# Kernel optimization log

Hardware: AMD Instinct MI355X
Metric: run time of the kernel (lower is better)

## Reference

```python
import jax, jax.numpy as jnp
import numpy as np

NEG_INF = jnp.float32(-1e30)


def setup_inputs() -> dict:
    key = jax.random.key(0)
    ks = jax.random.split(key, 7)
    B, Lx, Lm, d = 4, 256, 256, 256
    return {
        "x": jax.random.normal(ks[0], (B, Lx, d), dtype=jnp.float32),
        "memory": jax.random.normal(ks[1], (B, Lm, d), dtype=jnp.float32),
        "memory_mask": jax.random.randint(ks[2], (B, Lm), 0, 2, dtype=jnp.int32),
        "ws1_w": jax.random.normal(ks[3], (d, d), dtype=jnp.float32) * 0.05,
        "ws1_b": jax.random.normal(ks[4], (d,), dtype=jnp.float32) * 0.05,
        "ws2_w": jax.random.normal(ks[5], (d, d), dtype=jnp.float32) * 0.05,
        "wst_w": jax.random.normal(ks[6], (1, d), dtype=jnp.float32) * 0.05,
    }


def reference(x, memory, memory_mask, ws1_w, ws1_b, ws2_w, wst_w):
    # x: [B, Lx, d], memory: [B, Lm, d]; torch Linear: y = x @ W.T + b
    item1 = jnp.einsum('bxd,ed->bxe', x, ws1_w) + ws1_b          # [B, Lx, d]
    item2 = jnp.einsum('bmd,ed->bme', memory, ws2_w)             # [B, Lm, d]
    item = jnp.tanh(item1[:, :, None, :] + item2[:, None, :, :])  # [B, Lx, Lm, d]
    S = jnp.einsum('bxmd,d->bxm', item, wst_w[0])                # [B, Lx, Lm]
    # agg_2_h uses the UNMASKED scores, softmax over Lx after transpose
    agg_2_h = jnp.einsum('bmx,bxd->bmd', jax.nn.softmax(S.transpose(0, 2, 1), axis=-1), x)
    # mask applied to S before the main attention readout
    S = jnp.where(memory_mask[:, None, :] == 0, NEG_INF, S)      # [B, Lx, Lm]
    out = jnp.einsum('bxm,bmd->bxd', jax.nn.softmax(S, axis=-1), memory)
    return (out, S, agg_2_h)
```

## Files before the change

kernel.cpp:

```cpp
#include <hip/hip_runtime.h>

static constexpr int NB = 4;
static constexpr int L  = 256;
static constexpr int D  = 256;

__device__ __forceinline__ float fast_rcp(float x) {
#if __has_builtin(__builtin_amdgcn_rcpf)
    return __builtin_amdgcn_rcpf(x);
#else
    return 1.0f / x;
#endif
}

__device__ __forceinline__ float fast_exp(float x) {
#if __has_builtin(__builtin_amdgcn_exp2f)
    return __builtin_amdgcn_exp2f(x * 1.4426950408889634f);
#else
    return __expf(x);
#endif
}

__device__ __forceinline__ float exp_2x(float x) {
#if __has_builtin(__builtin_amdgcn_exp2f)
    return __builtin_amdgcn_exp2f(x * 2.8853900817779268f);
#else
    return __expf(2.0f * x);
#endif
}

__device__ __forceinline__ float tanh_from_e(float e) {
    return fmaf(-2.0f, fast_rcp(e + 1.0f), 1.0f);
}

__global__ __launch_bounds__(256) void linear_kernel(
    const float* __restrict__ x, const float* __restrict__ mem,
    const float* __restrict__ w1, const float* __restrict__ b1,
    const float* __restrict__ w2,
    float* __restrict__ E1X, float* __restrict__ E2X)
{
    const int bid = blockIdx.x;
    const int rb  = (bid >> 3) * 32;
    const int cb  = (bid & 7) * 32;
    const int which = rb >= 1024;
    const int rloc  = which ? rb - 1024 : rb;
    const float* src = which ? mem : x;
    const float* W   = which ? w2  : w1;
    float*       dstX = which ? E2X : E1X;

    constexpr int P4 = 65;
    __shared__ __align__(16) float4 xs4[32 * P4];
    __shared__ __align__(16) float4 ws4[32 * P4];

    const int t = threadIdx.x;
    const float4* src4 = reinterpret_cast<const float4*>(src) + rloc * 64;
    const float4* Wg4  = reinterpret_cast<const float4*>(W)   + cb   * 64;
#pragma unroll
    for (int k = 0; k < 8; ++k) {
        int idx = k * 256 + t;
        int r = idx >> 6, c = idx & 63;
        xs4[r * P4 + c] = src4[r * 64 + c];
        ws4[r * P4 + c] = Wg4[r * 64 + c];
    }
    __syncthreads();

    const int rr = t >> 4, cc = t & 15;
    const float4* a0p = xs4 + rr * P4;
    const float4* a1p = xs4 + (rr + 16) * P4;
    const float4* w0p = ws4 + cc * P4;
    const float4* w1p = ws4 + (cc + 16) * P4;
    float acc00 = 0.f, acc01 = 0.f, acc10 = 0.f, acc11 = 0.f;
#pragma unroll 4
    for (int d4 = 0; d4 < 64; ++d4) {
        float4 a0 = a0p[d4], a1 = a1p[d4];
        float4 w0 = w0p[d4], w1 = w1p[d4];
        acc00 = fmaf(a0.x, w0.x, acc00); acc00 = fmaf(a0.y, w0.y, acc00);
        acc00 = fmaf(a0.z, w0.z, acc00); acc00 = fmaf(a0.w, w0.w, acc00);
        acc01 = fmaf(a0.x, w1.x, acc01); acc01 = fmaf(a0.y, w1.y, acc01);
        acc01 = fmaf(a0.z, w1.z, acc01); acc01 = fmaf(a0.w, w1.w, acc01);
        acc10 = fmaf(a1.x, w0.x, acc10); acc10 = fmaf(a1.y, w0.y, acc10);
        acc10 = fmaf(a1.z, w0.z, acc10); acc10 = fmaf(a1.w, w0.w, acc10);
        acc11 = fmaf(a1.x, w1.x, acc11); acc11 = fmaf(a1.y, w1.y, acc11);
        acc11 = fmaf(a1.z, w1.z, acc11); acc11 = fmaf(a1.w, w1.w, acc11);
    }
    const float bias0 = which ? 0.f : b1[cb + cc];
    const float bias1 = which ? 0.f : b1[cb + cc + 16];
    const float e00 = exp_2x(acc00 + bias0);
    const float e01 = exp_2x(acc01 + bias1);
    const float e10 = exp_2x(acc10 + bias0);
    const float e11 = exp_2x(acc11 + bias1);
    const int c0 = cb + cc, c1 = cb + cc + 16;
    const int rA = rloc + rr, rB = rloc + rr + 16;
    dstX[((c0 >> 2) * 1024 + rA) * 4 + (c0 & 3)] = e00;
    dstX[((c1 >> 2) * 1024 + rA) * 4 + (c1 & 3)] = e01;
    dstX[((c0 >> 2) * 1024 + rB) * 4 + (c0 & 3)] = e10;
    dstX[((c1 >> 2) * 1024 + rB) * 4 + (c1 & 3)] = e11;
}

__global__ __launch_bounds__(256) void fused2_kernel(
    const float* __restrict__ x, const float* __restrict__ mem,
    const int* __restrict__ mask, const float* __restrict__ wst,
    const float* __restrict__ E1X, const float* __restrict__ E2X,
    float* __restrict__ out, float* __restrict__ Smask, float* __restrict__ agg)
{
    int bid = blockIdx.x;
    const bool isRow = bid < 256;
    if (!isRow) bid -= 256;
    const int b    = bid >> 6;
    const int r0   = (bid & 63) * 4;
    const int base = b * L;
    const int t    = threadIdx.x;

    const float4* laneE  = reinterpret_cast<const float4*>(isRow ? E2X : E1X);
    const float4* stripE = reinterpret_cast<const float4*>(isRow ? E1X : E2X);
    const float4* w4     = reinterpret_cast<const float4*>(wst);

    float acc0 = 0.f, acc1 = 0.f, acc2 = 0.f, acc3 = 0.f;
#pragma unroll 4
    for (int d4 = 0; d4 < 64; ++d4) {
        const int plane = d4 * 1024 + base;
        float4 ev = laneE[plane + t];
        float4 s0 = stripE[plane + r0];
        float4 s1 = stripE[plane + r0 + 1];
        float4 s2 = stripE[plane + r0 + 2];
        float4 s3 = stripE[plane + r0 + 3];
        float4 w  = w4[d4];
        acc0 = fmaf(tanh_from_e(ev.x * s0.x), w.x, acc0);
        acc0 = fmaf(tanh_from_e(ev.y * s0.y), w.y, acc0);
        acc0 = fmaf(tanh_from_e(ev.z * s0.z), w.z, acc0);
        acc0 = fmaf(tanh_from_e(ev.w * s0.w), w.w, acc0);
        acc1 = fmaf(tanh_from_e(ev.x * s1.x), w.x, acc1);
        acc1 = fmaf(tanh_from_e(ev.y * s1.y), w.y, acc1);
        acc1 = fmaf(tanh_from_e(ev.z * s1.z), w.z, acc1);
        acc1 = fmaf(tanh_from_e(ev.w * s1.w), w.w, acc1);
        acc2 = fmaf(tanh_from_e(ev.x * s2.x), w.x, acc2);
        acc2 = fmaf(tanh_from_e(ev.y * s2.y), w.y, acc2);
        acc2 = fmaf(tanh_from_e(ev.z * s2.z), w.z, acc2);
        acc2 = fmaf(tanh_from_e(ev.w * s2.w), w.w, acc2);
        acc3 = fmaf(tanh_from_e(ev.x * s3.x), w.x, acc3);
        acc3 = fmaf(tanh_from_e(ev.y * s3.y), w.y, acc3);
        acc3 = fmaf(tanh_from_e(ev.z * s3.z), w.z, acc3);
        acc3 = fmaf(tanh_from_e(ev.w * s3.w), w.w, acc3);
    }

    __shared__ __align__(16) float sS[4][L];
    __shared__ __align__(16) float4 part[4][4][64];

    if (isRow) {
        const bool dead = (mask[base + t] == 0);
        const float v0 = dead ? -1e30f : acc0;
        const float v1 = dead ? -1e30f : acc1;
        const float v2 = dead ? -1e30f : acc2;
        const float v3 = dead ? -1e30f : acc3;
        Smask[((base + r0 + 0) << 8) + t] = v0;
        Smask[((base + r0 + 1) << 8) + t] = v1;
        Smask[((base + r0 + 2) << 8) + t] = v2;
        Smask[((base + r0 + 3) << 8) + t] = v3;
        sS[0][t] = v0; sS[1][t] = v1; sS[2][t] = v2; sS[3][t] = v3;
    } else {
        sS[0][t] = acc0; sS[1][t] = acc1; sS[2][t] = acc2; sS[3][t] = acc3;
    }
    __syncthreads();

    const int w = t >> 6, l = t & 63;
    {
        float4 sv = reinterpret_cast<const float4*>(sS[w])[l];
        float m = fmaxf(fmaxf(sv.x, sv.y), fmaxf(sv.z, sv.w));
#pragma unroll
        for (int o = 32; o; o >>= 1) m = fmaxf(m, __shfl_xor(m, o));
        float e0 = fast_exp(sv.x - m), e1 = fast_exp(sv.y - m);
        float e2 = fast_exp(sv.z - m), e3 = fast_exp(sv.w - m);
        float s = (e0 + e1) + (e2 + e3);
#pragma unroll
        for (int o = 32; o; o >>= 1) s += __shfl_xor(s, o);
        float rs = fast_rcp(s);
        reinterpret_cast<float4*>(sS[w])[l] =
            make_float4(e0 * rs, e1 * rs, e2 * rs, e3 * rs);
    }
    __syncthreads();

    const float4* V4 = reinterpret_cast<const float4*>(isRow ? mem : x) + base * 64;
    float4 acc[4];
#pragma unroll
    for (int r = 0; r < 4; ++r) acc[r] = make_float4(0.f, 0.f, 0.f, 0.f);

#pragma unroll 2
    for (int k4 = 0; k4 < 16; ++k4) {
        const int m0 = w * 64 + k4 * 4;
        float4 v0 = V4[(m0 + 0) * 64 + l];
        float4 v1 = V4[(m0 + 1) * 64 + l];
        float4 v2 = V4[(m0 + 2) * 64 + l];
        float4 v3 = V4[(m0 + 3) * 64 + l];
#pragma unroll
        for (int r = 0; r < 4; ++r) {
            float4 pr = *reinterpret_cast<const float4*>(&sS[r][m0]);
            acc[r].x = fmaf(pr.x, v0.x, acc[r].x); acc[r].y = fmaf(pr.x, v0.y, acc[r].y);
            acc[r].z = fmaf(pr.x, v0.z, acc[r].z); acc[r].w = fmaf(pr.x, v0.w, acc[r].w);
            acc[r].x = fmaf(pr.y, v1.x, acc[r].x); acc[r].y = fmaf(pr.y, v1.y, acc[r].y);
            acc[r].z = fmaf(pr.y, v1.z, acc[r].z); acc[r].w = fmaf(pr.y, v1.w, acc[r].w);
            acc[r].x = fmaf(pr.z, v2.x, acc[r].x); acc[r].y = fmaf(pr.z, v2.y, acc[r].y);
            acc[r].z = fmaf(pr.z, v2.z, acc[r].z); acc[r].w = fmaf(pr.z, v2.w, acc[r].w);
            acc[r].x = fmaf(pr.w, v3.x, acc[r].x); acc[r].y = fmaf(pr.w, v3.y, acc[r].y);
            acc[r].z = fmaf(pr.w, v3.z, acc[r].z); acc[r].w = fmaf(pr.w, v3.w, acc[r].w);
        }
    }
#pragma unroll
    for (int r = 0; r < 4; ++r) part[r][w][l] = acc[r];
    __syncthreads();

    {
        float4 q0 = part[w][0][l], q1 = part[w][1][l];
        float4 q2 = part[w][2][l], q3 = part[w][3][l];
        float4 ov;
        ov.x = (q0.x + q1.x) + (q2.x + q3.x);
        ov.y = (q0.y + q1.y) + (q2.y + q3.y);
        ov.z = (q0.z + q1.z) + (q2.z + q3.z);
        ov.w = (q0.w + q1.w) + (q2.w + q3.w);
        float* o = isRow ? out : agg;
        reinterpret_cast<float4*>(o)[((base + r0 + w) << 6) + l] = ov;
    }
}

extern "C" void kernel_launch(void* const* d_in, const int* in_sizes, int n_in,
                              void* d_out, int out_size, void* d_ws, size_t ws_size,
                              hipStream_t stream)
{
    const float* x    = (const float*)d_in[0];
    const float* mem  = (const float*)d_in[1];
    const int*   mask = (const int*)  d_in[2];
    const float* w1   = (const float*)d_in[3];
    const float* b1   = (const float*)d_in[4];
    const float* w2   = (const float*)d_in[5];
    const float* wst  = (const float*)d_in[6];

    float* out   = (float*)d_out;
    float* Smask = out + NB * L * L;
    float* agg   = Smask + NB * L * L;

    float* E1X = (float*)d_ws;
    float* E2X = E1X + NB * L * D;

    linear_kernel<<<512, 256, 0, stream>>>(x, mem, w1, b1, w2, E1X, E2X);
    fused2_kernel<<<512, 256, 0, stream>>>(x, mem, mask, wst, E1X, E2X,
                                           out, Smask, agg);
}
```

Measured before the change: 42.82 us.

## Factor tanh weight sum out of score loop and stage strip rows in LDS

Rewrites the score sum using tanh(a)=1-2/(e+1), so the inner loop accumulates w*rcp(fma(e1,e2,1)) and the constant sum of w is added once afterwards. The linear kernel also writes a row-major copy of the exponentials, which the fused kernel stages with the weights into shared memory instead of issuing strided global loads per iteration. Softmax drops the max subtraction and defers normalization to the final output scale, which saves a reduction and a sync but can overflow exp for large scores. It adds extra workspace writes.

```diff
diff --git a/kernel.cpp b/kernel.cpp
--- a/kernel.cpp
+++ b/kernel.cpp
@@ -28,15 +28,12 @@
 #endif
 }
 
-__device__ __forceinline__ float tanh_from_e(float e) {
-    return fmaf(-2.0f, fast_rcp(e + 1.0f), 1.0f);
-}
-
 __global__ __launch_bounds__(256) void linear_kernel(
     const float* __restrict__ x, const float* __restrict__ mem,
     const float* __restrict__ w1, const float* __restrict__ b1,
     const float* __restrict__ w2,
-    float* __restrict__ E1X, float* __restrict__ E2X)
+    float* __restrict__ E1X, float* __restrict__ E2X,
+    float* __restrict__ E1R, float* __restrict__ E2R)
 {
     const int bid = blockIdx.x;
     const int rb  = (bid >> 3) * 32;
@@ -45,7 +42,8 @@
     const int rloc  = which ? rb - 1024 : rb;
     const float* src = which ? mem : x;
     const float* W   = which ? w2  : w1;
-    float*       dstX = which ? E2X : E1X;
+    float* dstX = which ? E2X : E1X;
+    float* dstR = which ? E2R : E1R;
 
     constexpr int P4 = 65;
     __shared__ __align__(16) float4 xs4[32 * P4];
@@ -94,12 +92,17 @@
     dstX[((c1 >> 2) * 1024 + rA) * 4 + (c1 & 3)] = e01;
     dstX[((c0 >> 2) * 1024 + rB) * 4 + (c0 & 3)] = e10;
     dstX[((c1 >> 2) * 1024 + rB) * 4 + (c1 & 3)] = e11;
+    dstR[rA * D + c0] = e00;
+    dstR[rA * D + c1] = e01;
+    dstR[rB * D + c0] = e10;
+    dstR[rB * D + c1] = e11;
 }
 
 __global__ __launch_bounds__(256) void fused2_kernel(
     const float* __restrict__ x, const float* __restrict__ mem,
     const int* __restrict__ mask, const float* __restrict__ wst,
     const float* __restrict__ E1X, const float* __restrict__ E2X,
+    const float* __restrict__ E1R, const float* __restrict__ E2R,
     float* __restrict__ out, float* __restrict__ Smask, float* __restrict__ agg)
 {
     int bid = blockIdx.x;
@@ -109,74 +112,89 @@
     const int r0   = (bid & 63) * 4;
     const int base = b * L;
     const int t    = threadIdx.x;
+    const int w    = t >> 6, l = t & 63;
 
     const float4* laneE  = reinterpret_cast<const float4*>(isRow ? E2X : E1X);
-    const float4* stripE = reinterpret_cast<const float4*>(isRow ? E1X : E2X);
-    const float4* w4     = reinterpret_cast<const float4*>(wst);
+    const float4* stripR = reinterpret_cast<const float4*>(isRow ? E1R : E2R);
+
+    __shared__ __align__(16) float4 sstrip[4][64];
+    __shared__ __align__(16) float4 swst[64];
+    __shared__ __align__(16) float  sS[4][L];
+    __shared__ __align__(16) float4 part[4][4][64];
+
+    {
+        int j = t >> 6, c = t & 63;
+        sstrip[j][c] = stripR[(base + r0 + j) * 64 + c];
+        if (t < 64) swst[t] = reinterpret_cast<const float4*>(wst)[t];
+    }
+    __syncthreads();
+
+    float W_tot;
+    {
+        float4 wv = swst[l];
+        float s = (wv.x + wv.y) + (wv.z + wv.w);
+#pragma unroll
+        for (int o = 32; o; o >>= 1) s += __shfl_xor(s, o);
+        W_tot = s;
+    }
 
     float acc0 = 0.f, acc1 = 0.f, acc2 = 0.f, acc3 = 0.f;
 #pragma unroll 4
     for (int d4 = 0; d4 < 64; ++d4) {
-        const int plane = d4 * 1024 + base;
-        float4 ev = laneE[plane + t];
-        float4 s0 = stripE[plane + r0];
-        float4 s1 = stripE[plane + r0 + 1];
-        float4 s2 = stripE[plane + r0 + 2];
-        float4 s3 = stripE[plane + r0 + 3];
-        float4 w  = w4[d4];
-        acc0 = fmaf(tanh_from_e(ev.x * s0.x), w.x, acc0);
-        acc0 = fmaf(tanh_from_e(ev.y * s0.y), w.y, acc0);
-        acc0 = fmaf(tanh_from_e(ev.z * s0.z), w.z, acc0);
-        acc0 = fmaf(tanh_from_e(ev.w * s0.w), w.w, acc0);
-        acc1 = fmaf(tanh_from_e(ev.x * s1.x), w.x, acc1);
-        acc1 = fmaf(tanh_from_e(ev.y * s1.y), w.y, acc1);
-        acc1 = fmaf(tanh_from_e(ev.z * s1.z), w.z, acc1);
-        acc1 = fmaf(tanh_from_e(ev.w * s1.w), w.w, acc1);
-        acc2 = fmaf(tanh_from_e(ev.x * s2.x), w.x, acc2);
-        acc2 = fmaf(tanh_from_e(ev.y * s2.y), w.y, acc2);
-        acc2 = fmaf(tanh_from_e(ev.z * s2.z), w.z, acc2);
-        acc2 = fmaf(tanh_from_e(ev.w * s2.w), w.w, acc2);
-        acc3 = fmaf(tanh_from_e(ev.x * s3.x), w.x, acc3);
-        acc3 = fmaf(tanh_from_e(ev.y * s3.y), w.y, acc3);
-        acc3 = fmaf(tanh_from_e(ev.z * s3.z), w.z, acc3);
-        acc3 = fmaf(tanh_from_e(ev.w * s3.w), w.w, acc3);
-    }
-
-    __shared__ __align__(16) float sS[4][L];
-    __shared__ __align__(16) float4 part[4][4][64];
+        float4 ev = laneE[d4 * 1024 + base + t];
+        float4 s0 = sstrip[0][d4];
+        float4 s1 = sstrip[1][d4];
+        float4 s2 = sstrip[2][d4];
+        float4 s3 = sstrip[3][d4];
+        float4 wv = swst[d4];
+        acc0 = fmaf(wv.x, fast_rcp(fmaf(ev.x, s0.x, 1.f)), acc0);
+        acc0 = fmaf(wv.y, fast_rcp(fmaf(ev.y, s0.y, 1.f)), acc0);
+        acc0 = fmaf(wv.z, fast_rcp(fmaf(ev.z, s0.z, 1.f)), acc0);
+        acc0 = fmaf(wv.w, fast_rcp(fmaf(ev.w, s0.w, 1.f)), acc0);
+        acc1 = fmaf(wv.x, fast_rcp(fmaf(ev.x, s1.x, 1.f)), acc1);
+        acc1 = fmaf(wv.y, fast_rcp(fmaf(ev.y, s1.y, 1.f)), acc1);
+        acc1 = fmaf(wv.z, fast_rcp(fmaf(ev.z, s1.z, 1.f)), acc1);
+        acc1 = fmaf(wv.w, fast_rcp(fmaf(ev.w, s1.w, 1.f)), acc1);
+        acc2 = fmaf(wv.x, fast_rcp(fmaf(ev.x, s2.x, 1.f)), acc2);
+        acc2 = fmaf(wv.y, fast_rcp(fmaf(ev.y, s2.y, 1.f)), acc2);
+        acc2 = fmaf(wv.z, fast_rcp(fmaf(ev.z, s2.z, 1.f)), acc2);
+        acc2 = fmaf(wv.w, fast_rcp(fmaf(ev.w, s2.w, 1.f)), acc2);
+        acc3 = fmaf(wv.x, fast_rcp(fmaf(ev.x, s3.x, 1.f)), acc3);
+        acc3 = fmaf(wv.y, fast_rcp(fmaf(ev.y, s3.y, 1.f)), acc3);
+        acc3 = fmaf(wv.z, fast_rcp(fmaf(ev.z, s3.z, 1.f)), acc3);
+        acc3 = fmaf(wv.w, fast_rcp(fmaf(ev.w, s3.w, 1.f)), acc3);
+    }
+    float S0 = fmaf(-2.f, acc0, W_tot);
+    float S1 = fmaf(-2.f, acc1, W_tot);
+    float S2 = fmaf(-2.f, acc2, W_tot);
+    float S3 = fmaf(-2.f, acc3, W_tot);
 
     if (isRow) {
         const bool dead = (mask[base + t] == 0);
-        const float v0 = dead ? -1e30f : acc0;
-        const float v1 = dead ? -1e30f : acc1;
-        const float v2 = dead ? -1e30f : acc2;
-        const float v3 = dead ? -1e30f : acc3;
-        Smask[((base + r0 + 0) << 8) + t] = v0;
-        Smask[((base + r0 + 1) << 8) + t] = v1;
-        Smask[((base + r0 + 2) << 8) + t] = v2;
-        Smask[((base + r0 + 3) << 8) + t] = v3;
-        sS[0][t] = v0; sS[1][t] = v1; sS[2][t] = v2; sS[3][t] = v3;
+        Smask[((base + r0 + 0) << 8) + t] = dead ? -1e30f : S0;
+        Smask[((base + r0 + 1) << 8) + t] = dead ? -1e30f : S1;
+        Smask[((base + r0 + 2) << 8) + t] = dead ? -1e30f : S2;
+        Smask[((base + r0 + 3) << 8) + t] = dead ? -1e30f : S3;
+        sS[0][t] = dead ? 0.f : fast_exp(S0);
+        sS[1][t] = dead ? 0.f : fast_exp(S1);
+        sS[2][t] = dead ? 0.f : fast_exp(S2);
+        sS[3][t] = dead ? 0.f : fast_exp(S3);
     } else {
-        sS[0][t] = acc0; sS[1][t] = acc1; sS[2][t] = acc2; sS[3][t] = acc3;
-    }
-    __syncthreads();
-
-    const int w = t >> 6, l = t & 63;
-    {
-        float4 sv = reinterpret_cast<const float4*>(sS[w])[l];
-        float m = fmaxf(fmaxf(sv.x, sv.y), fmaxf(sv.z, sv.w));
-#pragma unroll
-        for (int o = 32; o; o >>= 1) m = fmaxf(m, __shfl_xor(m, o));
-        float e0 = fast_exp(sv.x - m), e1 = fast_exp(sv.y - m);
-        float e2 = fast_exp(sv.z - m), e3 = fast_exp(sv.w - m);
-        float s = (e0 + e1) + (e2 + e3);
+        sS[0][t] = fast_exp(S0);
+        sS[1][t] = fast_exp(S1);
+        sS[2][t] = fast_exp(S2);
+        sS[3][t] = fast_exp(S3);
+    }
+    __syncthreads();
+
+    float rs_w;
+    {
+        float4 ev4 = reinterpret_cast<const float4*>(sS[w])[l];
+        float s = (ev4.x + ev4.y) + (ev4.z + ev4.w);
 #pragma unroll
         for (int o = 32; o; o >>= 1) s += __shfl_xor(s, o);
-        float rs = fast_rcp(s);
-        reinterpret_cast<float4*>(sS[w])[l] =
-            make_float4(e0 * rs, e1 * rs, e2 * rs, e3 * rs);
-    }
-    __syncthreads();
+        rs_w = fast_rcp(s);
+    }
 
     const float4* V4 = reinterpret_cast<const float4*>(isRow ? mem : x) + base * 64;
     float4 acc[4];
@@ -211,10 +229,10 @@
         float4 q0 = part[w][0][l], q1 = part[w][1][l];
         float4 q2 = part[w][2][l], q3 = part[w][3][l];
         float4 ov;
-        ov.x = (q0.x + q1.x) + (q2.x + q3.x);
-        ov.y = (q0.y + q1.y) + (q2.y + q3.y);
-        ov.z = (q0.z + q1.z) + (q2.z + q3.z);
-        ov.w = (q0.w + q1.w) + (q2.w + q3.w);
+        ov.x = ((q0.x + q1.x) + (q2.x + q3.x)) * rs_w;
+        ov.y = ((q0.y + q1.y) + (q2.y + q3.y)) * rs_w;
+        ov.z = ((q0.z + q1.z) + (q2.z + q3.z)) * rs_w;
+        ov.w = ((q0.w + q1.w) + (q2.w + q3.w)) * rs_w;
         float* o = isRow ? out : agg;
         reinterpret_cast<float4*>(o)[((base + r0 + w) << 6) + l] = ov;
     }
@@ -238,8 +256,10 @@
 
     float* E1X = (float*)d_ws;
     float* E2X = E1X + NB * L * D;
-
-    linear_kernel<<<512, 256, 0, stream>>>(x, mem, w1, b1, w2, E1X, E2X);
-    fused2_kernel<<<512, 256, 0, stream>>>(x, mem, mask, wst, E1X, E2X,
+    float* E1R = E2X + NB * L * D;
+    float* E2R = E1R + NB * L * D;
+
+    linear_kernel<<<512, 256, 0, stream>>>(x, mem, w1, b1, w2, E1X, E2X, E1R, E2R);
+    fused2_kernel<<<512, 256, 0, stream>>>(x, mem, mask, wst, E1X, E2X, E1R, E2R,
                                            out, Smask, agg);
 }
```

Result: faster. 41.70 us (-2.6%).
